# Performance work log

Hardware: AMD Instinct MI355X
Metric: run time of the kernel (lower is better)

## Reference

```python
import jax, jax.numpy as jnp
import numpy as np

COORD_W, EDGE_W, COUNT_W, REG_W, CONTRA_W = 1.0, 2.0, 0.1, 0.001, 0.1
MARGIN = 1.0


def setup_inputs() -> dict:
    key = jax.random.key(0)
    ks = jax.random.split(key, 6)
    B, N, D, C = 16, 1024, 128, 2
    return {
        "predicted_coords": jax.random.normal(ks[0], (B, N, C), jnp.float32),
        "points": jax.random.normal(ks[1], (B, N, C), jnp.float32),
        "adjacency_logits": jax.random.normal(ks[2], (B, N, N), jnp.float32),
        "adjacency": jax.random.bernoulli(ks[3], 0.1, (B, N, N)).astype(jnp.float32),
        "node_masks": jnp.ones((B, N), jnp.float32),  # all nodes valid -> n_actual = N
        "predicted_count": jax.random.normal(ks[4], (B, 1), jnp.float32),
        "node_features": jax.random.normal(ks[5], (B, N, D), jnp.float32),
    }


def _bce_with_logits(logits, targets):
    # mean-reduced, numerically stable (matches F.binary_cross_entropy_with_logits)
    return jnp.mean(jnp.maximum(logits, 0.0) - logits * targets
                    + jnp.log1p(jnp.exp(-jnp.abs(logits))))


def _smooth_l1(pred, target):
    d = jnp.abs(pred - target)
    return jnp.mean(jnp.where(d < 1.0, 0.5 * d * d, d - 0.5))


def _contrastive_sample(features, adj):
    # features: [N, D], adj: [N, N]. torch.cdist pairwise euclidean via gram trick.
    nrm = jnp.sum(features * features, axis=-1)              # [N]
    sq = jnp.maximum(nrm[:, None] + nrm[None, :]
                     - 2.0 * (features @ features.T), 0.0)   # [N, N] squared dists
    n = features.shape[0]
    eye = jnp.eye(n, dtype=bool)
    pos_mask = adj > 0.5
    neg_mask = (adj <= 0.5) & (~eye)
    # positive term: mean of distances**2 over positive pairs == mean squared dist
    pos = jnp.sum(jnp.where(pos_mask, sq, 0.0)) / jnp.maximum(jnp.sum(pos_mask), 1)
    dist = jnp.sqrt(jnp.maximum(sq, 1e-12))
    hinge = jnp.square(jax.nn.relu(MARGIN - dist))
    neg = jnp.sum(jnp.where(neg_mask, hinge, 0.0)) / jnp.maximum(jnp.sum(neg_mask), 1)
    return pos + neg


def reference(predicted_coords, points, adjacency_logits, adjacency,
              node_masks, predicted_count, node_features):
    # node_masks are all ones, so the per-sample [:n_actual] slicing is the
    # full tensor; per-sample MSE/BCE means averaged over batch equal global means.
    coord_loss = jnp.mean(jnp.square(predicted_coords - points))
    edge_loss = _bce_with_logits(adjacency_logits, adjacency)
    actual_counts = jnp.sum(node_masks, axis=1)              # [B]
    count_loss = _smooth_l1(predicted_count[:, 0], actual_counts)
    reg_loss = jnp.mean(jnp.square(node_features))
    # contrastive path uses targets['adjacency'] (no predicted_adjacency key)
    contra_loss = jnp.mean(jax.vmap(_contrastive_sample)(node_features, adjacency))
    total = (COORD_W * coord_loss + EDGE_W * edge_loss + COUNT_W * count_loss
             + REG_W * reg_loss + CONTRA_W * contra_loss)
    return total, coord_loss, edge_loss, count_loss, reg_loss, contra_loss
```

## Files before the change

### kernel.cpp

```cpp
#include <hip/hip_runtime.h>
#include <hip/hip_bf16.h>

#define NN    1024
#define DD    128
#define TILE  128
#define PITCH 136
#define SQP   132
#define NBLK  1024

typedef __bf16 bf16_t;
typedef bf16_t bf16x8 __attribute__((ext_vector_type(8)));
typedef float  f32x4  __attribute__((ext_vector_type(4)));


__global__ __launch_bounds__(256) void small_losses(
    const float* __restrict__ pcoord, const float* __restrict__ pts,
    const float* __restrict__ masks,  const float* __restrict__ pcount,
    float* __restrict__ ws) {
  __shared__ float sh[4][2];
  float coord = 0.f, cnt = 0.f;

  const int gt = blockIdx.x * 256 + threadIdx.x;
  const int stride = 16 * 256;

  const float4* a4 = (const float4*)pcoord;
  const float4* b4 = (const float4*)pts;
  for (int i = gt; i < 8192; i += stride) {
    float4 a = a4[i], b = b4[i];
    float dx = a.x-b.x, dy = a.y-b.y, dz = a.z-b.z, dw = a.w-b.w;
    coord += dx*dx + dy*dy + dz*dz + dw*dw;
  }
  const float* m = masks + blockIdx.x * NN;
  for (int i = threadIdx.x; i < NN; i += 256) cnt += m[i];

  const int lane = threadIdx.x & 63, w = threadIdx.x >> 6;
  #pragma unroll
  for (int o = 32; o; o >>= 1) {
    coord += __shfl_xor(coord, o);
    cnt   += __shfl_xor(cnt, o);
  }
  if (lane == 0) { sh[w][0] = coord; sh[w][1] = cnt; }
  __syncthreads();
  if (threadIdx.x == 0) {
    float c = 0.f, n = 0.f;
    for (int i = 0; i < 4; ++i) { c += sh[i][0]; n += sh[i][1]; }
    atomicAdd(&ws[0], c);
    float d = fabsf(pcount[blockIdx.x] - n);
    float term = (d < 1.f) ? 0.5f * d * d : d - 0.5f;
    atomicAdd(&ws[2], term);
  }
}

__device__ __forceinline__ void loss_elem(float l, float a, float s, int grow, int gcol,
    float& bsum, float& poss, float& posc, float& negs, float& negc) {
  bsum += fmaxf(l, 0.f) - l * a + __logf(1.f + __expf(-fabsf(l)));
  if (a > 0.5f) {
    poss += s; posc += 1.f;
  } else if (grow != gcol) {
    negc += 1.f;
    if (s < 1.f) {
      float d = sqrtf(fmaxf(s, 1e-12f));
      float h = 1.f - d;
      negs += h * h;
    }
  }
}

__global__ __launch_bounds__(512, 4) void fused_gram_bce(
    const float* __restrict__ logits, const float* __restrict__ adj,
    const float* __restrict__ feat, float* __restrict__ ws) {
  __shared__ __align__(16) char smem[2 * TILE * PITCH * sizeof(bf16_t)];
  bf16_t* lsA = (bf16_t*)smem;
  bf16_t* lsB = (bf16_t*)(smem + TILE * PITCH * sizeof(bf16_t));
  float*  sqb = (float*)smem;
  __shared__ float nrmA[TILE], nrmB[TILE];
  __shared__ float red[8][6];

  const int bx  = blockIdx.x;
  const int b   = bx >> 6;
  const int tid = bx & 63;
  const int ti  = (tid >> 3) << 7;
  const int tj  = (tid & 7)  << 7;
  const bool diag = ((tid >> 3) == (tid & 7));

  const int t = threadIdx.x;
  const float* fb = feat + (size_t)b * NN * DD;

  float regsum = 0.f;
  #pragma unroll
  for (int it = 0; it < 8; ++it) {
    int cid  = it * 512 + t;
    int tile = cid >> 11;
    int sub  = cid & 2047;
    int row  = sub >> 4;
    int c8   = sub & 15;
    const float* src = fb + (size_t)((tile ? tj : ti) + row) * DD + c8 * 8;
    float4 u = *(const float4*)src;
    float4 v = *(const float4*)(src + 4);
    if (diag && tile == 0)
      regsum += u.x*u.x + u.y*u.y + u.z*u.z + u.w*u.w
              + v.x*v.x + v.y*v.y + v.z*v.z + v.w*v.w;
    bf16_t* dst = (tile ? lsB : lsA) + row * PITCH + c8 * 8;
    dst[0] = (bf16_t)u.x; dst[1] = (bf16_t)u.y; dst[2] = (bf16_t)u.z; dst[3] = (bf16_t)u.w;
    dst[4] = (bf16_t)v.x; dst[5] = (bf16_t)v.y; dst[6] = (bf16_t)v.z; dst[7] = (bf16_t)v.w;
  }
  __syncthreads();

  {
    int row  = t >> 1;
    int half = t & 1;
    const bf16_t* src = (row < TILE ? lsA + row * PITCH : lsB + (row - TILE) * PITCH)
                        + half * 64;
    float s = 0.f;
    #pragma unroll
    for (int c = 0; c < 8; ++c) {
      bf16x8 ch = *(const bf16x8*)(src + c * 8);
      #pragma unroll
      for (int i = 0; i < 8; ++i) { float v = (float)ch[i]; s += v * v; }
    }
    s += __shfl_xor(s, 1);
    if (half == 0) { if (row < TILE) nrmA[row] = s; else nrmB[row - TILE] = s; }
  }

  const int lane = t & 63;
  const int wave = t >> 6;
  const int lrow = lane & 15;
  const int quad = lane >> 4;

  f32x4 acc[8];
  #pragma unroll
  for (int fc = 0; fc < 8; ++fc) acc[fc] = (f32x4){0.f, 0.f, 0.f, 0.f};

  #pragma unroll
  for (int k0 = 0; k0 < DD; k0 += 32) {
    const int kc = k0 + quad * 8;
    bf16x8 aF = *(const bf16x8*)&lsA[(wave * 16 + lrow) * PITCH + kc];
    bf16x8 bF[8];
    #pragma unroll
    for (int fc = 0; fc < 8; ++fc)
      bF[fc] = *(const bf16x8*)&lsB[(fc * 16 + lrow) * PITCH + kc];
    #pragma unroll
    for (int fc = 0; fc < 8; ++fc)
      acc[fc] = __builtin_amdgcn_mfma_f32_16x16x32_bf16(aF, bF[fc], acc[fc], 0, 0, 0);
  }

  const int c4 = t & 31, r0 = t >> 5;
  const int gcol0 = tj + c4 * 4;
  const size_t base = (size_t)b * NN * NN;
  const float* lp = logits + base + (size_t)(ti + r0) * NN + gcol0;
  const float* ap = adj    + base + (size_t)(ti + r0) * NN + gcol0;
  float4 Lb[8], Ab[8];
  #pragma unroll
  for (int i = 0; i < 8; ++i) {
    Lb[i] = *(const float4*)(lp + (size_t)i * 16 * NN);
    Ab[i] = *(const float4*)(ap + (size_t)i * 16 * NN);
  }

  __syncthreads();

  {
    const int rbase = wave * 16 + quad * 4;
    #pragma unroll
    for (int fc = 0; fc < 8; ++fc) {
      const int ctile = fc * 16 + lrow;
      const float ncol = nrmB[ctile];
      #pragma unroll
      for (int r = 0; r < 4; ++r) {
        const int rtile = rbase + r;
        sqb[rtile * SQP + ctile] = fmaxf(nrmA[rtile] + ncol - 2.f * acc[fc][r], 0.f);
      }
    }
  }
  __syncthreads();

  float bsum = 0.f, poss = 0.f, posc = 0.f, negs = 0.f, negc = 0.f;
  #pragma unroll
  for (int it = 0; it < 8; ++it) {
    const int row  = it * 16 + r0;
    const int grow = ti + row;
    float4 L = Lb[it], A = Ab[it];
    float4 s = *(const float4*)&sqb[row * SQP + c4 * 4];
    loss_elem(L.x, A.x, s.x, grow, gcol0 + 0, bsum, poss, posc, negs, negc);
    loss_elem(L.y, A.y, s.y, grow, gcol0 + 1, bsum, poss, posc, negs, negc);
    loss_elem(L.z, A.z, s.z, grow, gcol0 + 2, bsum, poss, posc, negs, negc);
    loss_elem(L.w, A.w, s.w, grow, gcol0 + 3, bsum, poss, posc, negs, negc);
  }

  #pragma unroll
  for (int o = 32; o; o >>= 1) {
    bsum   += __shfl_xor(bsum, o);
    poss   += __shfl_xor(poss, o);
    posc   += __shfl_xor(posc, o);
    negs   += __shfl_xor(negs, o);
    negc   += __shfl_xor(negc, o);
    regsum += __shfl_xor(regsum, o);
  }
  if (lane == 0) {
    red[wave][0] = bsum; red[wave][1] = poss; red[wave][2] = posc;
    red[wave][3] = negs; red[wave][4] = negc; red[wave][5] = regsum;
  }
  __syncthreads();
  if (t == 0) {
    float s0=0.f,s1=0.f,s2=0.f,s3=0.f,s4=0.f,s5=0.f;
    for (int w = 0; w < 8; ++w) {
      s0 += red[w][0]; s1 += red[w][1]; s2 += red[w][2];
      s3 += red[w][3]; s4 += red[w][4]; s5 += red[w][5];
    }
    atomicAdd(&ws[3], s0);
    atomicAdd(&ws[4 + b], s1);
    atomicAdd(&ws[20 + b], s2);
    atomicAdd(&ws[36 + b], s3);
    atomicAdd(&ws[52 + b], s4);
    if (diag) atomicAdd(&ws[1], s5);
  }
}

__global__ void finalize(const float* __restrict__ ws, float* __restrict__ out) {
  if (threadIdx.x != 0 || blockIdx.x != 0) return;
  float coord = ws[0] / 32768.f;
  float reg   = ws[1] / 2097152.f;
  float cntl  = ws[2] / 16.f;
  float edge  = ws[3] / 16777216.f;
  float contra = 0.f;
  for (int b = 0; b < 16; ++b) {
    float p = ws[4 + b]  / fmaxf(ws[20 + b], 1.f);
    float n = ws[36 + b] / fmaxf(ws[52 + b], 1.f);
    contra += p + n;
  }
  contra *= (1.f / 16.f);
  float total = coord + 2.f * edge + 0.1f * cntl + 0.001f * reg + 0.1f * contra;
  out[0] = total; out[1] = coord; out[2] = edge;
  out[3] = cntl;  out[4] = reg;   out[5] = contra;
}

extern "C" void kernel_launch(void* const* d_in, const int* in_sizes, int n_in,
                              void* d_out, int out_size, void* d_ws, size_t ws_size,
                              hipStream_t stream) {
  (void)in_sizes; (void)n_in; (void)out_size; (void)ws_size;
  const float* pcoord = (const float*)d_in[0];
  const float* pts    = (const float*)d_in[1];
  const float* logits = (const float*)d_in[2];
  const float* adj    = (const float*)d_in[3];
  const float* masks  = (const float*)d_in[4];
  const float* pcount = (const float*)d_in[5];
  const float* nf     = (const float*)d_in[6];
  float* ws  = (float*)d_ws;
  float* out = (float*)d_out;

  hipMemsetAsync(ws, 0, 68 * sizeof(float), stream);
  small_losses<<<16, 256, 0, stream>>>(pcoord, pts, masks, pcount, ws);
  fused_gram_bce<<<NBLK, 512, 0, stream>>>(logits, adj, nf, ws);
  finalize<<<1, 64, 0, stream>>>(ws, out);
}
```

Baseline: 200.7 us.

## Use 64x64 gram tiles, consume MFMA results in registers, merge small-loss kernel

Shrinks the per-block tile from 128x128 to 64x64 with 256 threads and a 4096-block grid. The squared-distance tile no longer goes through an LDS staging buffer: each lane reads the logits and adjacency elements matching its MFMA accumulator layout and evaluates the loss in registers. The small-losses kernel is folded into the same launch as 16 extra blocks, and bf16 LDS stores are packed into one vector store. This removes an LDS round trip, a barrier and a launch, but the global loads become scalar 4-byte loads strided by 16 columns, and the 64x64 tiles reload more feature data per output element.

```diff
diff --git a/kernel.cpp b/kernel.cpp
--- a/kernel.cpp
+++ b/kernel.cpp
@@ -3,53 +3,16 @@
 
 #define NN    1024
 #define DD    128
-#define TILE  128
+#define TS    64
 #define PITCH 136
-#define SQP   132
-#define NBLK  1024
+#define NSMALL 16
+#define GRID_MAIN 4096
+#define GRID_ALL  4112
 
 typedef __bf16 bf16_t;
 typedef bf16_t bf16x8 __attribute__((ext_vector_type(8)));
 typedef float  f32x4  __attribute__((ext_vector_type(4)));
 
-
-__global__ __launch_bounds__(256) void small_losses(
-    const float* __restrict__ pcoord, const float* __restrict__ pts,
-    const float* __restrict__ masks,  const float* __restrict__ pcount,
-    float* __restrict__ ws) {
-  __shared__ float sh[4][2];
-  float coord = 0.f, cnt = 0.f;
-
-  const int gt = blockIdx.x * 256 + threadIdx.x;
-  const int stride = 16 * 256;
-
-  const float4* a4 = (const float4*)pcoord;
-  const float4* b4 = (const float4*)pts;
-  for (int i = gt; i < 8192; i += stride) {
-    float4 a = a4[i], b = b4[i];
-    float dx = a.x-b.x, dy = a.y-b.y, dz = a.z-b.z, dw = a.w-b.w;
-    coord += dx*dx + dy*dy + dz*dz + dw*dw;
-  }
-  const float* m = masks + blockIdx.x * NN;
-  for (int i = threadIdx.x; i < NN; i += 256) cnt += m[i];
-
-  const int lane = threadIdx.x & 63, w = threadIdx.x >> 6;
-  #pragma unroll
-  for (int o = 32; o; o >>= 1) {
-    coord += __shfl_xor(coord, o);
-    cnt   += __shfl_xor(cnt, o);
-  }
-  if (lane == 0) { sh[w][0] = coord; sh[w][1] = cnt; }
-  __syncthreads();
-  if (threadIdx.x == 0) {
-    float c = 0.f, n = 0.f;
-    for (int i = 0; i < 4; ++i) { c += sh[i][0]; n += sh[i][1]; }
-    atomicAdd(&ws[0], c);
-    float d = fabsf(pcount[blockIdx.x] - n);
-    float term = (d < 1.f) ? 0.5f * d * d : d - 0.5f;
-    atomicAdd(&ws[2], term);
-  }
-}
 
 __device__ __forceinline__ void loss_elem(float l, float a, float s, int grow, int gcol,
     float& bsum, float& poss, float& posc, float& negs, float& negc) {
@@ -66,32 +29,68 @@
   }
 }
 
-__global__ __launch_bounds__(512, 4) void fused_gram_bce(
+__global__ __launch_bounds__(256, 4) void fused_all(
     const float* __restrict__ logits, const float* __restrict__ adj,
-    const float* __restrict__ feat, float* __restrict__ ws) {
-  __shared__ __align__(16) char smem[2 * TILE * PITCH * sizeof(bf16_t)];
-  bf16_t* lsA = (bf16_t*)smem;
-  bf16_t* lsB = (bf16_t*)(smem + TILE * PITCH * sizeof(bf16_t));
-  float*  sqb = (float*)smem;
-  __shared__ float nrmA[TILE], nrmB[TILE];
-  __shared__ float red[8][6];
-
-  const int bx  = blockIdx.x;
-  const int b   = bx >> 6;
-  const int tid = bx & 63;
-  const int ti  = (tid >> 3) << 7;
-  const int tj  = (tid & 7)  << 7;
-  const bool diag = ((tid >> 3) == (tid & 7));
-
-  const int t = threadIdx.x;
+    const float* __restrict__ feat,
+    const float* __restrict__ pcoord, const float* __restrict__ pts,
+    const float* __restrict__ masks,  const float* __restrict__ pcount,
+    float* __restrict__ ws) {
+  __shared__ __align__(16) bf16_t lsA[TS * PITCH];
+  __shared__ __align__(16) bf16_t lsB[TS * PITCH];
+  __shared__ float nrmA[TS], nrmB[TS];
+  __shared__ float red[4][6];
+
+  const int bx = blockIdx.x;
+  const int t  = threadIdx.x;
+
+  if (bx < NSMALL) {
+    float coord = 0.f, cnt = 0.f;
+    const int gt = bx * 256 + t;
+    const float4* a4 = (const float4*)pcoord;
+    const float4* b4 = (const float4*)pts;
+    for (int i = gt; i < 8192; i += 4096) {
+      float4 a = a4[i], c = b4[i];
+      float dx = a.x-c.x, dy = a.y-c.y, dz = a.z-c.z, dw = a.w-c.w;
+      coord += dx*dx + dy*dy + dz*dz + dw*dw;
+    }
+    const float* m = masks + bx * NN;
+    for (int i = t; i < NN; i += 256) cnt += m[i];
+    #pragma unroll
+    for (int o = 32; o; o >>= 1) {
+      coord += __shfl_xor(coord, o);
+      cnt   += __shfl_xor(cnt, o);
+    }
+    const int lane = t & 63, w = t >> 6;
+    if (lane == 0) { red[w][0] = coord; red[w][1] = cnt; }
+    __syncthreads();
+    if (t == 0) {
+      float c = 0.f, n = 0.f;
+      for (int i = 0; i < 4; ++i) { c += red[i][0]; n += red[i][1]; }
+      atomicAdd(&ws[0], c);
+      float d = fabsf(pcount[bx] - n);
+      float term = (d < 1.f) ? 0.5f * d * d : d - 0.5f;
+      atomicAdd(&ws[2], term);
+    }
+    return;
+  }
+
+  const int bm  = bx - NSMALL;
+  const int b   = bm >> 8;
+  const int tid = bm & 255;
+  const int ti  = (tid >> 4) << 6;
+  const int tj  = (tid & 15) << 6;
+  const bool diag = ((tid >> 4) == (tid & 15));
+
+  const int lane = t & 63, wave = t >> 6;
+  const int lrow = lane & 15, quad = lane >> 4;
   const float* fb = feat + (size_t)b * NN * DD;
 
   float regsum = 0.f;
   #pragma unroll
   for (int it = 0; it < 8; ++it) {
-    int cid  = it * 512 + t;
-    int tile = cid >> 11;
-    int sub  = cid & 2047;
+    int cid  = it * 256 + t;
+    int tile = cid >> 10;
+    int sub  = cid & 1023;
     int row  = sub >> 4;
     int c8   = sub & 15;
     const float* src = fb + (size_t)((tile ? tj : ti) + row) * DD + c8 * 8;
@@ -100,16 +99,32 @@
     if (diag && tile == 0)
       regsum += u.x*u.x + u.y*u.y + u.z*u.z + u.w*u.w
               + v.x*v.x + v.y*v.y + v.z*v.z + v.w*v.w;
-    bf16_t* dst = (tile ? lsB : lsA) + row * PITCH + c8 * 8;
-    dst[0] = (bf16_t)u.x; dst[1] = (bf16_t)u.y; dst[2] = (bf16_t)u.z; dst[3] = (bf16_t)u.w;
-    dst[4] = (bf16_t)v.x; dst[5] = (bf16_t)v.y; dst[6] = (bf16_t)v.z; dst[7] = (bf16_t)v.w;
+    bf16x8 pk;
+    pk[0]=(bf16_t)u.x; pk[1]=(bf16_t)u.y; pk[2]=(bf16_t)u.z; pk[3]=(bf16_t)u.w;
+    pk[4]=(bf16_t)v.x; pk[5]=(bf16_t)v.y; pk[6]=(bf16_t)v.z; pk[7]=(bf16_t)v.w;
+    *(bf16x8*)((tile ? lsB : lsA) + row * PITCH + c8 * 8) = pk;
   }
   __syncthreads();
 
+  const size_t tb = (size_t)b * NN * NN
+                  + (size_t)(ti + wave * 16 + quad * 4) * NN + (tj + lrow);
+  const float* lp = logits + tb;
+  const float* ap = adj + tb;
+  float Lv[4][4], Av[4][4];
+  #pragma unroll
+  for (int r = 0; r < 4; ++r) {
+    const float* lr = lp + (size_t)r * NN;
+    const float* ar = ap + (size_t)r * NN;
+    #pragma unroll
+    for (int fc = 0; fc < 4; ++fc) {
+      Lv[fc][r] = lr[fc * 16];
+      Av[fc][r] = ar[fc * 16];
+    }
+  }
+
   {
-    int row  = t >> 1;
-    int half = t & 1;
-    const bf16_t* src = (row < TILE ? lsA + row * PITCH : lsB + (row - TILE) * PITCH)
+    int row = t >> 1, half = t & 1;
+    const bf16_t* src = (row < TS ? lsA + row * PITCH : lsB + (row - TS) * PITCH)
                         + half * 64;
     float s = 0.f;
     #pragma unroll
@@ -119,71 +134,41 @@
       for (int i = 0; i < 8; ++i) { float v = (float)ch[i]; s += v * v; }
     }
     s += __shfl_xor(s, 1);
-    if (half == 0) { if (row < TILE) nrmA[row] = s; else nrmB[row - TILE] = s; }
-  }
-
-  const int lane = t & 63;
-  const int wave = t >> 6;
-  const int lrow = lane & 15;
-  const int quad = lane >> 4;
-
-  f32x4 acc[8];
-  #pragma unroll
-  for (int fc = 0; fc < 8; ++fc) acc[fc] = (f32x4){0.f, 0.f, 0.f, 0.f};
-
+    if (half == 0) { if (row < TS) nrmA[row] = s; else nrmB[row - TS] = s; }
+  }
+
+  f32x4 acc[4];
+  #pragma unroll
+  for (int fc = 0; fc < 4; ++fc) acc[fc] = (f32x4){0.f, 0.f, 0.f, 0.f};
   #pragma unroll
   for (int k0 = 0; k0 < DD; k0 += 32) {
     const int kc = k0 + quad * 8;
     bf16x8 aF = *(const bf16x8*)&lsA[(wave * 16 + lrow) * PITCH + kc];
-    bf16x8 bF[8];
-    #pragma unroll
-    for (int fc = 0; fc < 8; ++fc)
-      bF[fc] = *(const bf16x8*)&lsB[(fc * 16 + lrow) * PITCH + kc];
-    #pragma unroll
-    for (int fc = 0; fc < 8; ++fc)
-      acc[fc] = __builtin_amdgcn_mfma_f32_16x16x32_bf16(aF, bF[fc], acc[fc], 0, 0, 0);
-  }
-
-  const int c4 = t & 31, r0 = t >> 5;
-  const int gcol0 = tj + c4 * 4;
-  const size_t base = (size_t)b * NN * NN;
-  const float* lp = logits + base + (size_t)(ti + r0) * NN + gcol0;
-  const float* ap = adj    + base + (size_t)(ti + r0) * NN + gcol0;
-  float4 Lb[8], Ab[8];
-  #pragma unroll
-  for (int i = 0; i < 8; ++i) {
-    Lb[i] = *(const float4*)(lp + (size_t)i * 16 * NN);
-    Ab[i] = *(const float4*)(ap + (size_t)i * 16 * NN);
-  }
-
+    #pragma unroll
+    for (int fc = 0; fc < 4; ++fc) {
+      bf16x8 bF = *(const bf16x8*)&lsB[(fc * 16 + lrow) * PITCH + kc];
+      acc[fc] = __builtin_amdgcn_mfma_f32_16x16x32_bf16(aF, bF, acc[fc], 0, 0, 0);
+    }
+  }
   __syncthreads();
 
-  {
-    const int rbase = wave * 16 + quad * 4;
-    #pragma unroll
-    for (int fc = 0; fc < 8; ++fc) {
-      const int ctile = fc * 16 + lrow;
-      const float ncol = nrmB[ctile];
-      #pragma unroll
-      for (int r = 0; r < 4; ++r) {
-        const int rtile = rbase + r;
-        sqb[rtile * SQP + ctile] = fmaxf(nrmA[rtile] + ncol - 2.f * acc[fc][r], 0.f);
-      }
-    }
-  }
-  __syncthreads();
+  float nA[4], nB[4];
+  #pragma unroll
+  for (int r = 0; r < 4; ++r) nA[r] = nrmA[wave * 16 + quad * 4 + r];
+  #pragma unroll
+  for (int fc = 0; fc < 4; ++fc) nB[fc] = nrmB[fc * 16 + lrow];
 
   float bsum = 0.f, poss = 0.f, posc = 0.f, negs = 0.f, negc = 0.f;
-  #pragma unroll
-  for (int it = 0; it < 8; ++it) {
-    const int row  = it * 16 + r0;
-    const int grow = ti + row;
-    float4 L = Lb[it], A = Ab[it];
-    float4 s = *(const float4*)&sqb[row * SQP + c4 * 4];
-    loss_elem(L.x, A.x, s.x, grow, gcol0 + 0, bsum, poss, posc, negs, negc);
-    loss_elem(L.y, A.y, s.y, grow, gcol0 + 1, bsum, poss, posc, negs, negc);
-    loss_elem(L.z, A.z, s.z, grow, gcol0 + 2, bsum, poss, posc, negs, negc);
-    loss_elem(L.w, A.w, s.w, grow, gcol0 + 3, bsum, poss, posc, negs, negc);
+  const int grow0 = ti + wave * 16 + quad * 4;
+  const int gcol0 = tj + lrow;
+  #pragma unroll
+  for (int fc = 0; fc < 4; ++fc) {
+    #pragma unroll
+    for (int r = 0; r < 4; ++r) {
+      float s = fmaxf(nA[r] + nB[fc] - 2.f * acc[fc][r], 0.f);
+      loss_elem(Lv[fc][r], Av[fc][r], s, grow0 + r, gcol0 + fc * 16,
+                bsum, poss, posc, negs, negc);
+    }
   }
 
   #pragma unroll
@@ -202,7 +187,7 @@
   __syncthreads();
   if (t == 0) {
     float s0=0.f,s1=0.f,s2=0.f,s3=0.f,s4=0.f,s5=0.f;
-    for (int w = 0; w < 8; ++w) {
+    for (int w = 0; w < 4; ++w) {
       s0 += red[w][0]; s1 += red[w][1]; s2 += red[w][2];
       s3 += red[w][3]; s4 += red[w][4]; s5 += red[w][5];
     }
@@ -248,7 +233,6 @@
   float* out = (float*)d_out;
 
   hipMemsetAsync(ws, 0, 68 * sizeof(float), stream);
-  small_losses<<<16, 256, 0, stream>>>(pcoord, pts, masks, pcount, ws);
-  fused_gram_bce<<<NBLK, 512, 0, stream>>>(logits, adj, nf, ws);
+  fused_all<<<GRID_ALL, 256, 0, stream>>>(logits, adj, nf, pcoord, pts, masks, pcount, ws);
   finalize<<<1, 64, 0, stream>>>(ws, out);
 }
```

New measurement: 263.1 us. 1.31x slower.
